# Kernel tuning notes

Hardware: AMD Instinct MI355X
Metric: run time of the kernel (lower is better)

## Reference

```python
import jax, jax.numpy as jnp
import numpy as np

B, L, C, H, S = 32, 4096, 512, 8, 8
NW = L // S          # slide_num = 512 windows
D = C // H           # head dim = 64


def setup_inputs() -> dict:
    key = jax.random.key(0)
    ks = jax.random.split(key, 6)
    p = lambda k, sh: jax.random.normal(k, sh, jnp.float32) * 0.02
    return {
        'x': jax.random.normal(ks[0], (B, L, C), jnp.float32),
        'Wq': p(ks[1], (C, C)), 'bq': jnp.zeros((C,), jnp.float32),
        'Wk': p(ks[2], (C, C)), 'bk': jnp.zeros((C,), jnp.float32),
        'Wv': p(ks[3], (C, C)), 'bv': jnp.zeros((C,), jnp.float32),
        'Wp': p(ks[4], (C, C)), 'bp': jnp.zeros((C,), jnp.float32),
        'bias_table': p(ks[5], (2 * S - 1, H)),  # trunc_normal(std=0.02) analogue
    }


def _shift_mask():
    # Swin-style shift mask: segment ids 0 / 1 / 2 over the last window's halves.
    seg = np.zeros(L, np.float32)
    seg[L - S:L - S // 2] = 1.0
    seg[L - S // 2:] = 2.0
    mw = seg.reshape(NW, S)                       # [NW, S]
    diff = mw[:, :, None] - mw[:, None, :]        # [NW, S, S]
    return jnp.asarray(np.where(diff != 0, -100.0, 0.0), jnp.float32)


def reference(x, Wq, bq, Wk, bk, Wv, bv, Wp, bp, bias_table):
    # shift=True: roll left by S//2, window, attend, unwindow, roll back
    xs = jnp.roll(x, -S // 2, axis=1).reshape(B * NW, S, C)

    def heads(w, b):
        return (xs @ w + b).reshape(B * NW, S, H, D).transpose(0, 2, 1, 3)

    q, k, v = heads(Wq, bq), heads(Wk, bk), heads(Wv, bv)
    # NOTE: original scales by sqrt(emb_size), not sqrt(head_dim)
    energy = jnp.einsum('bhqd,bhkd->bhqk', q, k) / jnp.sqrt(jnp.float32(C))

    # relative position bias: index[i, j] = j - i + S - 1
    idx = jnp.arange(S)[None, :] - jnp.arange(S)[:, None] + (S - 1)
    bias = bias_table[idx].transpose(2, 0, 1)     # [H, S, S]
    energy = energy + bias[None]

    mask = _shift_mask()                          # [NW, S, S]
    energy = energy.reshape(B, NW, H, S, S) + mask[None, :, None]
    att = jax.nn.softmax(energy, axis=-1).reshape(B * NW, H, S, S)

    out = jnp.einsum('bhqk,bhkd->bhqd', att, v)
    out = out.transpose(0, 2, 1, 3).reshape(B * NW, S, C)
    out = out @ Wp + bp
    return jnp.roll(out.reshape(B, L, C), S // 2, axis=1)
```

## Files before the change

### kernel.cpp

```cpp
#include <hip/hip_runtime.h>
#include <stdint.h>
#include <type_traits>


typedef unsigned short ushort_t;
typedef __bf16 v8bf __attribute__((ext_vector_type(8)));
typedef float v4f __attribute__((ext_vector_type(4)));

__device__ __forceinline__ ushort_t f2bf(float f) {
  unsigned int u = __float_as_uint(f);
  u = u + 0x7fffu + ((u >> 16) & 1u);
  return (ushort_t)(u >> 16);
}

__global__ __launch_bounds__(256) void prep_kernel(
    const float* __restrict__ Wq, const float* __restrict__ Wk,
    const float* __restrict__ Wv, const float* __restrict__ Wp,
    const float* __restrict__ bq, const float* __restrict__ bk,
    const float* __restrict__ bv,
    ushort_t* __restrict__ WTqkv, ushort_t* __restrict__ WTp,
    float* __restrict__ bqkvf)
{
  int idx = blockIdx.x * 256 + threadIdx.x;
  if (idx < 786432) {
    int n = idx % 1536;
    int k = idx / 1536;
    const float* W = (n < 512) ? Wq : (n < 1024) ? Wk : Wv;
    WTqkv[(size_t)n * 512 + k] = f2bf(W[k * 512 + (n & 511)]);
  } else if (idx < 1048576) {
    int j = idx - 786432;
    int n = j & 511;
    int k = j >> 9;
    WTp[(size_t)n * 512 + k] = f2bf(Wp[k * 512 + n]);
  } else if (idx < 1050112) {
    int n = idx - 1048576;
    const float* bb = (n < 512) ? bq : (n < 1024) ? bk : bv;
    bqkvf[n] = bb[n & 511];
  }
}

__global__ __launch_bounds__(256) void convert_roll_kernel(
    const float* __restrict__ x, ushort_t* __restrict__ xb)
{
  const int t = blockIdx.x * 256 + threadIdx.x;
  const int m = t >> 6;
  const int ch = t & 63;
  const int b = m >> 12;
  const int r = m & 4095;
  const int src = (b << 12) | ((r + 4) & 4095);
  const float4* p = (const float4*)(x + (size_t)src * 512 + ch * 8);
  float4 a0 = p[0], a1 = p[1];
  uint4 o;
  o.x = (unsigned)f2bf(a0.x) | ((unsigned)f2bf(a0.y) << 16);
  o.y = (unsigned)f2bf(a0.z) | ((unsigned)f2bf(a0.w) << 16);
  o.z = (unsigned)f2bf(a1.x) | ((unsigned)f2bf(a1.y) << 16);
  o.w = (unsigned)f2bf(a1.z) | ((unsigned)f2bf(a1.w) << 16);
  *(uint4*)(xb + (size_t)m * 512 + ch * 8) = o;
}


#define SB() __builtin_amdgcn_sched_barrier(0)

__device__ __forceinline__ void stage_half(
    const ushort_t* __restrict__ G, ushort_t* lds_b, int boff,
    int kt, int half, int rowbase, int tid)
{
  ushort_t* Lb = lds_b + boff + (((kt & 1) << 1) + half) * 8192;
  const int rb = rowbase + (half << 7);
#pragma unroll
  for (int i = 0; i < 2; ++i) {
    const int c = tid + (i << 9);
    const int row = c >> 3;
    const int slot = c & 7;
    const int scol = (slot ^ (row & 7)) << 3;
    const ushort_t* src = G + (size_t)(rb + row) * 512 + (kt << 6) + scol;
    __builtin_amdgcn_global_load_lds(
        (const __attribute__((address_space(1))) void*)src,
        (__attribute__((address_space(3))) void*)(Lb + ((size_t)c << 3)),
        16, 0, 0);
  }
}

__device__ __forceinline__ void mfma_quad(
    v4f (&accq)[2][4], const v8bf (&af)[2][2], const v8bf (&bq)[4][2])
{
#pragma unroll
  for (int mi = 0; mi < 2; ++mi)
#pragma unroll
    for (int ni = 0; ni < 4; ++ni)
#pragma unroll
      for (int kk = 0; kk < 2; ++kk)
        accq[mi][ni] = __builtin_amdgcn_mfma_f32_16x16x32_bf16(
            af[mi][kk], bq[ni][kk], accq[mi][ni], 0, 0, 0);
}

template<int LDC, int GN, bool ROLL_C, typename OutT>
__global__ __launch_bounds__(512)
__attribute__((amdgpu_waves_per_eu(2, 2)))
void gemm256(
    const ushort_t* __restrict__ A, const ushort_t* __restrict__ BT,
    const float* __restrict__ bias, OutT* __restrict__ C)
{
  extern __shared__ ushort_t lds[];

  const int tid = threadIdx.x;
  const int l   = tid & 63;
  const int wv  = tid >> 6;
  const int wr  = wv >> 1;
  const int wc  = wv & 1;
  const int fr  = l & 15;
  const int fq  = l >> 4;

  constexpr int NWG = GN * 512;
  const int bid = blockIdx.x;
  const int swz = (bid & 7) * (NWG >> 3) + (bid >> 3);
  const int m0 = (swz / GN) * 256;
  const int n0 = (swz % GN) * 256;

  const int arow = wr * 32 + fr;
  const int brow = wc * 64 + fr;
  const int kswz = (fr & 7) << 3;
  const int kb   = fq << 3;

#define LDA_FRAGS(bufq) do { \
  _Pragma("unroll") for (int mi = 0; mi < 2; ++mi) \
  _Pragma("unroll") for (int kk = 0; kk < 2; ++kk) \
    af[mi][kk] = *(const v8bf*)(lds + (bufq) * 8192 + \
        (arow + mi * 16) * 64 + ((kk * 32 + kb) ^ kswz)); \
} while (0)
#define LDB_FRAGS(qn, bufq) do { \
  _Pragma("unroll") for (int ni = 0; ni < 4; ++ni) \
  _Pragma("unroll") for (int kk = 0; kk < 2; ++kk) \
    bfr[qn][ni][kk] = *(const v8bf*)(lds + 32768 + (bufq) * 8192 + \
        (brow + ni * 16) * 64 + ((kk * 32 + kb) ^ kswz)); \
} while (0)
#define MFMA_PHASE(QM, QN) do { \
  SB(); __builtin_amdgcn_s_barrier(); SB(); \
  __builtin_amdgcn_s_setprio(1); \
  mfma_quad(acc[QM][QN], af, bfr[QN]); \
  __builtin_amdgcn_s_setprio(0); \
  SB(); } while (0)
#define ENDBAR() do { __builtin_amdgcn_s_barrier(); SB(); } while (0)

  v4f acc[2][2][2][4];
#pragma unroll
  for (int a = 0; a < 2; ++a)
#pragma unroll
    for (int b = 0; b < 2; ++b)
#pragma unroll
      for (int m = 0; m < 2; ++m)
#pragma unroll
        for (int n = 0; n < 4; ++n)
          acc[a][b][m][n] = (v4f){0.f, 0.f, 0.f, 0.f};

  stage_half(A,  lds, 0,     0, 0, m0, tid);
  stage_half(BT, lds, 32768, 0, 0, n0, tid);
  stage_half(A,  lds, 0,     0, 1, m0, tid);
  stage_half(BT, lds, 32768, 0, 1, n0, tid);
  stage_half(A,  lds, 0,     1, 0, m0, tid);
  stage_half(BT, lds, 32768, 1, 0, n0, tid);
  SB();
  asm volatile("s_waitcnt vmcnt(4)" ::: "memory");
  __builtin_amdgcn_s_barrier();
  SB();

  for (int t = 0; t < 4; ++t) {
    const bool more = (t < 3);
    const int o = 2 * t + 1;
    v8bf af[2][2];
    v8bf bfr[2][4][2];

    LDA_FRAGS(0);
    LDB_FRAGS(0, 0);
    stage_half(A, lds, 0, o, 1, m0, tid);
    MFMA_PHASE(0, 0);
    ENDBAR();
    LDB_FRAGS(1, 1);
    stage_half(BT, lds, 32768, o, 1, n0, tid);
    MFMA_PHASE(0, 1);
    ENDBAR();
    LDA_FRAGS(1);
    if (more) stage_half(A, lds, 0, o + 1, 0, m0, tid);
    MFMA_PHASE(1, 0);
    ENDBAR();
    if (more) stage_half(BT, lds, 32768, o + 1, 0, n0, tid);
    MFMA_PHASE(1, 1);
    if (t == 3) asm volatile("s_waitcnt vmcnt(0)" ::: "memory");
    else        asm volatile("s_waitcnt vmcnt(4)" ::: "memory");
    ENDBAR();
    LDA_FRAGS(2);
    LDB_FRAGS(0, 2);
    if (more) stage_half(A, lds, 0, o + 1, 1, m0, tid);
    MFMA_PHASE(0, 0);
    ENDBAR();
    LDB_FRAGS(1, 3);
    if (more) stage_half(BT, lds, 32768, o + 1, 1, n0, tid);
    MFMA_PHASE(0, 1);
    ENDBAR();
    LDA_FRAGS(3);
    if (more) stage_half(A, lds, 0, o + 2, 0, m0, tid);
    MFMA_PHASE(1, 0);
    ENDBAR();
    if (more) stage_half(BT, lds, 32768, o + 2, 0, n0, tid);
    MFMA_PHASE(1, 1);
    asm volatile("s_waitcnt vmcnt(4)" ::: "memory");
    ENDBAR();
  }

#pragma unroll
  for (int Qm = 0; Qm < 2; ++Qm)
#pragma unroll
    for (int Qn = 0; Qn < 2; ++Qn)
#pragma unroll
      for (int mi = 0; mi < 2; ++mi)
#pragma unroll
        for (int ni = 0; ni < 4; ++ni) {
          const int col = n0 + Qn * 128 + wc * 64 + ni * 16 + fr;
          const float bv = bias[col];
#pragma unroll
          for (int r = 0; r < 4; ++r) {
            int row = m0 + Qm * 128 + wr * 32 + mi * 16 + fq * 4 + r;
            if (ROLL_C) row = (row & ~4095) | ((row + 4) & 4095);
            const float val = acc[Qm][Qn][mi][ni][r] + bv;
            if constexpr (std::is_same_v<OutT, float>)
              C[(size_t)row * LDC + col] = val;
            else
              C[(size_t)row * LDC + col] = f2bf(val);
          }
        }

#undef LDA_FRAGS
#undef LDB_FRAGS
#undef MFMA_PHASE
#undef ENDBAR
}

__device__ __forceinline__ void unpack8(uint4 v, float* f) {
  f[0] = __uint_as_float(v.x << 16); f[1] = __uint_as_float(v.x & 0xffff0000u);
  f[2] = __uint_as_float(v.y << 16); f[3] = __uint_as_float(v.y & 0xffff0000u);
  f[4] = __uint_as_float(v.z << 16); f[5] = __uint_as_float(v.z & 0xffff0000u);
  f[6] = __uint_as_float(v.w << 16); f[7] = __uint_as_float(v.w & 0xffff0000u);
}

__global__ __launch_bounds__(256) void attn_kernel(
    const ushort_t* __restrict__ qkv, const float* __restrict__ bias_table,
    ushort_t* __restrict__ attout)
{
  __shared__ float btab[120];
  if (threadIdx.x < 120) btab[threadIdx.x] = bias_table[threadIdx.x];
  __syncthreads();

  const int l  = threadIdx.x & 63;
  const int wv = threadIdx.x >> 6;
  const int u  = blockIdx.x * 4 + wv;
  const int b  = u >> 12;
  const int w  = (u >> 3) & 511;
  const int h  = u & 7;
  const int i  = l >> 3;
  const int c  = l & 7;

  const size_t rowi = (size_t)(b << 12) + (w << 3) + i;
  const ushort_t* pq = qkv + rowi * 1536 + h * 64 + c * 8;
  uint4 q8 = *(const uint4*)pq;
  uint4 k8 = *(const uint4*)(pq + 512);
  uint4 v8 = *(const uint4*)(pq + 1024);

  float qf[8];
  unpack8(q8, qf);

  float e[8];
#pragma unroll
  for (int t = 0; t < 8; ++t) {
    const int src = (l + 8 * t) & 63;
    uint4 kc;
    kc.x = __shfl((int)k8.x, src); kc.y = __shfl((int)k8.y, src);
    kc.z = __shfl((int)k8.z, src); kc.w = __shfl((int)k8.w, src);
    float kf[8]; unpack8(kc, kf);
    float s = 0.f;
#pragma unroll
    for (int d = 0; d < 8; ++d) s = fmaf(qf[d], kf[d], s);
    s += __shfl_xor(s, 1);
    s += __shfl_xor(s, 2);
    s += __shfl_xor(s, 4);
    e[t] = s;
  }

  const float scale = 0.044194173824159216f;
#pragma unroll
  for (int t = 0; t < 8; ++t) {
    const int j = (i + t) & 7;
    float ev = e[t] * scale + btab[(j - i + 7) * 8 + h];
    if (w == 511 && ((i < 4) != (j < 4))) ev -= 100.f;
    e[t] = ev;
  }

  float mx = e[0];
#pragma unroll
  for (int t = 1; t < 8; ++t) mx = fmaxf(mx, e[t]);
  float p[8], sum = 0.f;
#pragma unroll
  for (int t = 0; t < 8; ++t) { p[t] = __expf(e[t] - mx); sum += p[t]; }
  const float inv = __fdividef(1.f, sum);

  float of[8] = {0.f, 0.f, 0.f, 0.f, 0.f, 0.f, 0.f, 0.f};
#pragma unroll
  for (int t = 0; t < 8; ++t) {
    const int src = (l + 8 * t) & 63;
    uint4 vc;
    vc.x = __shfl((int)v8.x, src); vc.y = __shfl((int)v8.y, src);
    vc.z = __shfl((int)v8.z, src); vc.w = __shfl((int)v8.w, src);
    float vf[8]; unpack8(vc, vf);
    const float a = p[t] * inv;
#pragma unroll
    for (int d = 0; d < 8; ++d) of[d] = fmaf(a, vf[d], of[d]);
  }

  uint4 o;
  o.x = (unsigned)f2bf(of[0]) | ((unsigned)f2bf(of[1]) << 16);
  o.y = (unsigned)f2bf(of[2]) | ((unsigned)f2bf(of[3]) << 16);
  o.z = (unsigned)f2bf(of[4]) | ((unsigned)f2bf(of[5]) << 16);
  o.w = (unsigned)f2bf(of[6]) | ((unsigned)f2bf(of[7]) << 16);
  *(uint4*)(attout + rowi * 512 + h * 64 + c * 8) = o;
}

extern "C" void kernel_launch(void* const* d_in, const int* in_sizes, int n_in,
                              void* d_out, int out_size, void* d_ws, size_t ws_size,
                              hipStream_t stream) {
  (void)in_sizes; (void)n_in; (void)out_size; (void)ws_size;
  const float* x  = (const float*)d_in[0];
  const float* Wq = (const float*)d_in[1];
  const float* bq = (const float*)d_in[2];
  const float* Wk = (const float*)d_in[3];
  const float* bk = (const float*)d_in[4];
  const float* Wv = (const float*)d_in[5];
  const float* bv = (const float*)d_in[6];
  const float* Wp = (const float*)d_in[7];
  const float* bp = (const float*)d_in[8];
  const float* bt = (const float*)d_in[9];

  char* ws = (char*)d_ws;
  ushort_t* qkv    = (ushort_t*)(ws);
  ushort_t* xb     = (ushort_t*)(ws + 402653184ull);
  ushort_t* attout = xb;
  ushort_t* WTqkv  = (ushort_t*)(ws + 536870912ull);
  ushort_t* WTp    = (ushort_t*)(ws + 538443776ull);
  float*    bqkvf  = (float*)  (ws + 538968064ull);

  prep_kernel<<<4103, 256, 0, stream>>>(Wq, Wk, Wv, Wp, bq, bk, bv,
                                        WTqkv, WTp, bqkvf);
  convert_roll_kernel<<<32768, 256, 0, stream>>>(x, xb);
  gemm256<1536, 6, false, ushort_t><<<3072, 512, 131072, stream>>>(
      xb, WTqkv, bqkvf, qkv);
  attn_kernel<<<32768, 256, 0, stream>>>(qkv, bt, attout);
  gemm256<512, 2, true, float><<<1024, 512, 131072, stream>>>(
      attout, WTp, bp, (float*)d_out);
}
```

Measured before the change: 1.045 ms.

## Make GEMM blocks persistent over N tiles, streaming weights continuously

Each GEMM workgroup now owns one 256-row M tile and loops over all N tiles, so the grid shrinks to 512 blocks. The global-to-LDS pipeline continues across N-tile boundaries, and accumulators are written out and zeroed after each N tile. The intent is to keep the A rows hot in cache across N tiles and to avoid refilling the pipeline for every tile. In exchange, 512 blocks may underfill the GPU at two waves per EU, and the bid swizzle that improved cache locality is dropped.

```diff
diff --git a/kernel.cpp b/kernel.cpp
--- a/kernel.cpp
+++ b/kernel.cpp
@@ -63,9 +63,9 @@
 
 __device__ __forceinline__ void stage_half(
     const ushort_t* __restrict__ G, ushort_t* lds_b, int boff,
-    int kt, int half, int rowbase, int tid)
-{
-  ushort_t* Lb = lds_b + boff + (((kt & 1) << 1) + half) * 8192;
+    int g, int half, int rowbase, int tid)
+{
+  ushort_t* Lb = lds_b + boff + (((g & 1) << 1) + half) * 8192;
   const int rb = rowbase + (half << 7);
 #pragma unroll
   for (int i = 0; i < 2; ++i) {
@@ -73,7 +73,7 @@
     const int row = c >> 3;
     const int slot = c & 7;
     const int scol = (slot ^ (row & 7)) << 3;
-    const ushort_t* src = G + (size_t)(rb + row) * 512 + (kt << 6) + scol;
+    const ushort_t* src = G + (size_t)(rb + row) * 512 + ((g & 7) << 6) + scol;
     __builtin_amdgcn_global_load_lds(
         (const __attribute__((address_space(1))) void*)src,
         (__attribute__((address_space(3))) void*)(Lb + ((size_t)c << 3)),
@@ -111,16 +111,14 @@
   const int fr  = l & 15;
   const int fq  = l >> 4;
 
-  constexpr int NWG = GN * 512;
-  const int bid = blockIdx.x;
-  const int swz = (bid & 7) * (NWG >> 3) + (bid >> 3);
-  const int m0 = (swz / GN) * 256;
-  const int n0 = (swz % GN) * 256;
+  const int m0 = blockIdx.x << 8;
 
   const int arow = wr * 32 + fr;
   const int brow = wc * 64 + fr;
   const int kswz = (fr & 7) << 3;
   const int kb   = fq << 3;
+
+#define NB(g) ((((g) >> 3)) << 8)
 
 #define LDA_FRAGS(bufq) do { \
   _Pragma("unroll") for (int mi = 0; mi < 2; ++mi) \
@@ -154,81 +152,86 @@
           acc[a][b][m][n] = (v4f){0.f, 0.f, 0.f, 0.f};
 
   stage_half(A,  lds, 0,     0, 0, m0, tid);
-  stage_half(BT, lds, 32768, 0, 0, n0, tid);
+  stage_half(BT, lds, 32768, 0, 0, NB(0), tid);
   stage_half(A,  lds, 0,     0, 1, m0, tid);
-  stage_half(BT, lds, 32768, 0, 1, n0, tid);
+  stage_half(BT, lds, 32768, 0, 1, NB(0), tid);
   stage_half(A,  lds, 0,     1, 0, m0, tid);
-  stage_half(BT, lds, 32768, 1, 0, n0, tid);
+  stage_half(BT, lds, 32768, 1, 0, NB(1), tid);
   SB();
   asm volatile("s_waitcnt vmcnt(4)" ::: "memory");
   __builtin_amdgcn_s_barrier();
   SB();
 
-  for (int t = 0; t < 4; ++t) {
-    const bool more = (t < 3);
-    const int o = 2 * t + 1;
-    v8bf af[2][2];
-    v8bf bfr[2][4][2];
-
-    LDA_FRAGS(0);
-    LDB_FRAGS(0, 0);
-    stage_half(A, lds, 0, o, 1, m0, tid);
-    MFMA_PHASE(0, 0);
-    ENDBAR();
-    LDB_FRAGS(1, 1);
-    stage_half(BT, lds, 32768, o, 1, n0, tid);
-    MFMA_PHASE(0, 1);
-    ENDBAR();
-    LDA_FRAGS(1);
-    if (more) stage_half(A, lds, 0, o + 1, 0, m0, tid);
-    MFMA_PHASE(1, 0);
-    ENDBAR();
-    if (more) stage_half(BT, lds, 32768, o + 1, 0, n0, tid);
-    MFMA_PHASE(1, 1);
-    if (t == 3) asm volatile("s_waitcnt vmcnt(0)" ::: "memory");
-    else        asm volatile("s_waitcnt vmcnt(4)" ::: "memory");
-    ENDBAR();
-    LDA_FRAGS(2);
-    LDB_FRAGS(0, 2);
-    if (more) stage_half(A, lds, 0, o + 1, 1, m0, tid);
-    MFMA_PHASE(0, 0);
-    ENDBAR();
-    LDB_FRAGS(1, 3);
-    if (more) stage_half(BT, lds, 32768, o + 1, 1, n0, tid);
-    MFMA_PHASE(0, 1);
-    ENDBAR();
-    LDA_FRAGS(3);
-    if (more) stage_half(A, lds, 0, o + 2, 0, m0, tid);
-    MFMA_PHASE(1, 0);
-    ENDBAR();
-    if (more) stage_half(BT, lds, 32768, o + 2, 0, n0, tid);
-    MFMA_PHASE(1, 1);
-    asm volatile("s_waitcnt vmcnt(4)" ::: "memory");
-    ENDBAR();
-  }
-
-#pragma unroll
-  for (int Qm = 0; Qm < 2; ++Qm)
-#pragma unroll
-    for (int Qn = 0; Qn < 2; ++Qn)
-#pragma unroll
-      for (int mi = 0; mi < 2; ++mi)
-#pragma unroll
-        for (int ni = 0; ni < 4; ++ni) {
-          const int col = n0 + Qn * 128 + wc * 64 + ni * 16 + fr;
-          const float bv = bias[col];
-#pragma unroll
-          for (int r = 0; r < 4; ++r) {
-            int row = m0 + Qm * 128 + wr * 32 + mi * 16 + fq * 4 + r;
-            if (ROLL_C) row = (row & ~4095) | ((row + 4) & 4095);
-            const float val = acc[Qm][Qn][mi][ni][r] + bv;
-            if constexpr (std::is_same_v<OutT, float>)
-              C[(size_t)row * LDC + col] = val;
-            else
-              C[(size_t)row * LDC + col] = f2bf(val);
+  for (int nt = 0; nt < GN; ++nt) {
+    for (int t = 0; t < 4; ++t) {
+      const bool more = !(nt == GN - 1 && t == 3);
+      const int g1 = 8 * nt + 2 * t + 1;
+      v8bf af[2][2];
+      v8bf bfr[2][4][2];
+
+      LDA_FRAGS(0);
+      LDB_FRAGS(0, 0);
+      stage_half(A, lds, 0, g1, 1, m0, tid);
+      MFMA_PHASE(0, 0);
+      ENDBAR();
+      LDB_FRAGS(1, 1);
+      stage_half(BT, lds, 32768, g1, 1, NB(g1), tid);
+      MFMA_PHASE(0, 1);
+      ENDBAR();
+      LDA_FRAGS(1);
+      if (more) stage_half(A, lds, 0, g1 + 1, 0, m0, tid);
+      MFMA_PHASE(1, 0);
+      ENDBAR();
+      if (more) stage_half(BT, lds, 32768, g1 + 1, 0, NB(g1 + 1), tid);
+      MFMA_PHASE(1, 1);
+      if (more) asm volatile("s_waitcnt vmcnt(4)" ::: "memory");
+      else      asm volatile("s_waitcnt vmcnt(0)" ::: "memory");
+      ENDBAR();
+      LDA_FRAGS(2);
+      LDB_FRAGS(0, 2);
+      if (more) stage_half(A, lds, 0, g1 + 1, 1, m0, tid);
+      MFMA_PHASE(0, 0);
+      ENDBAR();
+      LDB_FRAGS(1, 3);
+      if (more) stage_half(BT, lds, 32768, g1 + 1, 1, NB(g1 + 1), tid);
+      MFMA_PHASE(0, 1);
+      ENDBAR();
+      LDA_FRAGS(3);
+      if (more) stage_half(A, lds, 0, g1 + 2, 0, m0, tid);
+      MFMA_PHASE(1, 0);
+      ENDBAR();
+      if (more) stage_half(BT, lds, 32768, g1 + 2, 0, NB(g1 + 2), tid);
+      MFMA_PHASE(1, 1);
+      asm volatile("s_waitcnt vmcnt(4)" ::: "memory");
+      ENDBAR();
+    }
+
+    const int n0t = nt << 8;
+#pragma unroll
+    for (int Qm = 0; Qm < 2; ++Qm)
+#pragma unroll
+      for (int Qn = 0; Qn < 2; ++Qn)
+#pragma unroll
+        for (int mi = 0; mi < 2; ++mi)
+#pragma unroll
+          for (int ni = 0; ni < 4; ++ni) {
+            const int col = n0t + Qn * 128 + wc * 64 + ni * 16 + fr;
+            const float bv = bias[col];
+#pragma unroll
+            for (int r = 0; r < 4; ++r) {
+              int row = m0 + Qm * 128 + wr * 32 + mi * 16 + fq * 4 + r;
+              if (ROLL_C) row = (row & ~4095) | ((row + 4) & 4095);
+              const float val = acc[Qm][Qn][mi][ni][r] + bv;
+              if constexpr (std::is_same_v<OutT, float>)
+                C[(size_t)row * LDC + col] = val;
+              else
+                C[(size_t)row * LDC + col] = f2bf(val);
+              acc[Qm][Qn][mi][ni][r] = 0.f;
+            }
           }
-        }
-
+  }
+
+#undef NB
 #undef LDA_FRAGS
 #undef LDB_FRAGS
 #undef MFMA_PHASE
@@ -349,9 +352,9 @@
   prep_kernel<<<4103, 256, 0, stream>>>(Wq, Wk, Wv, Wp, bq, bk, bv,
                                         WTqkv, WTp, bqkvf);
   convert_roll_kernel<<<32768, 256, 0, stream>>>(x, xb);
-  gemm256<1536, 6, false, ushort_t><<<3072, 512, 131072, stream>>>(
+  gemm256<1536, 6, false, ushort_t><<<512, 512, 131072, stream>>>(
       xb, WTqkv, bqkvf, qkv);
   attn_kernel<<<32768, 256, 0, stream>>>(qkv, bt, attout);
-  gemm256<512, 2, true, float><<<1024, 512, 131072, stream>>>(
+  gemm256<512, 2, true, float><<<512, 512, 131072, stream>>>(
       attout, WTp, bp, (float*)d_out);
 }
```

Measured after the change: 1.337 ms. +28.0%, slower.
